# Optimization experiments

Measured on AMD Instinct MI355X. Metric: run time of the kernel, lower is better.

The kernel has to match this reference:

```python
import jax, jax.numpy as jnp
import numpy as np

N = 30000   # nodes
E = 600000  # edges (avg degree 20)
H = 128     # hidden_channels
L = 4       # num_layers
G = 64      # graphs in batch


def _init(key, shape, fan_in):
    return (jax.random.normal(key, shape, jnp.float32) / np.sqrt(fan_in)).astype(jnp.float32)


def setup_inputs() -> dict:
    key = jax.random.key(0)
    ks = jax.random.split(key, 24)
    x = jax.random.normal(ks[0], (N, 1), jnp.float32)
    pos = jax.random.normal(ks[1], (N, 3), jnp.float32)
    edge_index = jax.random.randint(ks[2], (2, E), 0, N, dtype=jnp.int32).astype(jnp.int64)
    batch = jnp.sort(jax.random.randint(ks[3], (N,), 0, G, dtype=jnp.int32)).astype(jnp.int64)

    emb_w = _init(ks[4], (1, H), 1)
    emb_b = jnp.zeros((H,), jnp.float32)

    # stacked per-layer params: msg MLP (2H+1 -> H -> H), node MLP (2H -> H -> H)
    msg_w1 = _init(ks[5], (L, 2 * H + 1, H), 2 * H + 1)
    msg_b1 = jnp.zeros((L, H), jnp.float32)
    msg_w2 = _init(ks[6], (L, H, H), H)
    msg_b2 = jnp.zeros((L, H), jnp.float32)
    node_w1 = _init(ks[7], (L, 2 * H, H), 2 * H)
    node_b1 = jnp.zeros((L, H), jnp.float32)
    node_w2 = _init(ks[8], (L, H, H), H)
    node_b2 = jnp.zeros((L, H), jnp.float32)

    out_w1 = _init(ks[9], (H, 32), H)
    out_b1 = jnp.zeros((32,), jnp.float32)
    out_w2 = _init(ks[10], (32, 1), 32)
    out_b2 = jnp.zeros((1,), jnp.float32)

    return {
        "x": x, "pos": pos, "edge_index": edge_index, "batch": batch,
        "emb_w": emb_w, "emb_b": emb_b,
        "msg_w1": msg_w1, "msg_b1": msg_b1, "msg_w2": msg_w2, "msg_b2": msg_b2,
        "node_w1": node_w1, "node_b1": node_b1, "node_w2": node_w2, "node_b2": node_b2,
        "out_w1": out_w1, "out_b1": out_b1, "out_w2": out_w2, "out_b2": out_b2,
    }


def reference(x, pos, edge_index, batch,
              emb_w, emb_b,
              msg_w1, msg_b1, msg_w2, msg_b2,
              node_w1, node_b1, node_w2, node_b2,
              out_w1, out_b1, out_w2, out_b2):
    row, col = edge_index[0], edge_index[1]  # row = source j, col = target i
    # edge scalar: squared distance (computed once, reused across layers)
    dist_sq = jnp.sum((pos[row] - pos[col]) ** 2, axis=-1, keepdims=True)  # [E,1]

    h = x @ emb_w + emb_b  # [N,H]
    for l in range(L):
        x_j = h[row]   # source features
        x_i = h[col]   # target features
        m = jnp.concatenate([x_i, x_j, dist_sq], axis=-1)           # [E, 2H+1]
        m = jax.nn.silu(m @ msg_w1[l] + msg_b1[l]) @ msg_w2[l] + msg_b2[l]  # [E,H]
        aggr = jax.ops.segment_sum(m, col, num_segments=N)          # scatter-add to targets
        nh = jnp.concatenate([h, aggr], axis=-1)                    # [N, 2H]
        h = jax.nn.silu(nh @ node_w1[l] + node_b1[l]) @ node_w2[l] + node_b2[l]
        # dropout omitted for deterministic reference (eval mode)

    g = jax.ops.segment_sum(h, batch, num_segments=G)               # global_add_pool [G,H]
    return jax.nn.silu(g @ out_w1 + out_b1) @ out_w2 + out_b2       # [G,1]
```

## Files before the change

### kernel.cpp

```cpp
#include <hip/hip_runtime.h>

typedef unsigned short u16;
typedef __bf16 bf16x8 __attribute__((ext_vector_type(8)));
typedef float f32x4 __attribute__((ext_vector_type(4)));

#define HN 128
#define TM 64
#define ASTRIDE 136
#define ECH 256

__device__ __forceinline__ u16 f2bf(float f) {
  union { float f; unsigned u; } v; v.f = f;
  unsigned r = v.u + 0x7fffu + ((v.u >> 16) & 1u);
  return (u16)(r >> 16);
}
__device__ __forceinline__ float bf2f(u16 v) {
  union { unsigned u; float f; } x; x.u = ((unsigned)v) << 16; return x.f;
}
__device__ __forceinline__ float bflo(unsigned v) {
  union { unsigned u; float f; } x; x.u = v << 16; return x.f;
}
__device__ __forceinline__ float bfhi(unsigned v) {
  union { unsigned u; float f; } x; x.u = v & 0xffff0000u; return x.f;
}
__device__ __forceinline__ float silu_f(float x) {
  float e = __builtin_amdgcn_exp2f(-1.442695041f * x);
  return x * __builtin_amdgcn_rcpf(1.f + e);
}

__global__ void pack_weights(const float* __restrict__ msg_w1, const float* __restrict__ msg_w2,
                             const float* __restrict__ node_w1, const float* __restrict__ node_w2,
                             u16* __restrict__ pw, int* __restrict__ deg,
                             float* __restrict__ g, int N_, int GH) {
  int id = blockIdx.x * 256 + threadIdx.x;
  if (id < N_) deg[id] = 0;
  if (id < GH) g[id] = 0.f;
  if (id >= 4 * 6 * 16384) return;
  int l = id / (6 * 16384);
  int rem = id % (6 * 16384);
  int m = rem / 16384;
  int e = rem % 16384;
  int kg = e >> 10;
  int n = (e >> 3) & 127;
  int j = e & 7;
  int k = kg * 8 + j;
  float v = 0.f;
  switch (m) {
    case 0: v = msg_w1[(l * 257 + k) * 128 + n]; break;
    case 1: v = msg_w1[(l * 257 + 128 + k) * 128 + n]; break;
    case 2: v = msg_w2[(l * 128 + k) * 128 + n]; break;
    case 3: v = node_w1[(l * 256 + k) * 128 + n]; break;
    case 4: v = node_w1[(l * 256 + 128 + k) * 128 + n]; break;
    case 5: v = node_w2[(l * 128 + k) * 128 + n]; break;
  }
  pw[id] = f2bf(v);
}

__device__ __forceinline__ void gemm64(const u16* s_A, const u16* s_W,
                                       int w, int quad, int m16, f32x4 acc[8]) {
#pragma unroll
  for (int ks = 0; ks < 4; ks++) {
    bf16x8 a = *(const bf16x8*)&s_A[(w * 16 + m16) * ASTRIDE + ks * 32 + quad * 8];
#pragma unroll
    for (int ct = 0; ct < 8; ct++) {
      bf16x8 b = *(const bf16x8*)&s_W[(ks * 4 + quad) * 1024 + (ct * 16 + m16) * 8];
      acc[ct] = __builtin_amdgcn_mfma_f32_16x16x32_bf16(a, b, acc[ct], 0, 0, 0);
    }
  }
}

__global__ __launch_bounds__(256) void fold_kernel(
    const float* __restrict__ msg_w2, const float* __restrict__ node_w1,
    const float* __restrict__ msg_b2, const u16* __restrict__ pw,
    u16* __restrict__ pwc, float* __restrict__ vc) {
  __shared__ __align__(16) u16 s_A[TM * ASTRIDE];
  __shared__ __align__(16) u16 s_W[16384];
  const int t = threadIdx.x;
  const int w = t >> 6, lane = t & 63, quad = lane >> 4, m16 = lane & 15;
  const int b = blockIdx.x, l = b >> 1, half = b & 1;
  const int tile0 = half * 64;

  {
    int r = t >> 2, qo = (t & 3) * 32;
    const float4* src = (const float4*)(msg_w2 + (size_t)(l * 128 + tile0 + r) * 128 + qo);
    u16* dst = s_A + r * ASTRIDE + qo;
#pragma unroll
    for (int i = 0; i < 8; i++) {
      float4 v = src[i];
      ushort4 o;
      o.x = f2bf(v.x); o.y = f2bf(v.y); o.z = f2bf(v.z); o.w = f2bf(v.w);
      *(ushort4*)(dst + i * 4) = o;
    }
  }
  {
    const int4* src = (const int4*)(pw + (size_t)(l * 6 + 4) * 16384);
    int4* dst = (int4*)s_W;
#pragma unroll
    for (int i = 0; i < 8; i++) dst[t + i * 256] = src[t + i * 256];
  }
  __syncthreads();
  f32x4 acc[8];
#pragma unroll
  for (int ct = 0; ct < 8; ct++) acc[ct] = {0.f, 0.f, 0.f, 0.f};
  gemm64(s_A, s_W, w, quad, m16, acc);
#pragma unroll
  for (int ct = 0; ct < 8; ct++)
#pragma unroll
    for (int j = 0; j < 4; j++) {
      int k = tile0 + w * 16 + quad * 4 + j;
      int n = ct * 16 + m16;
      pwc[(size_t)l * 16384 + (k >> 3) * 1024 + n * 8 + (k & 7)] = f2bf(acc[ct][j]);
    }
  if (half == 0 && t < 128) {
    float s = 0.f;
    for (int np = 0; np < 128; np++)
      s += msg_b2[l * 128 + np] * node_w1[(size_t)(l * 256 + 128 + np) * 128 + t];
    vc[l * 128 + t] = s;
  }
}

__global__ void hist_kernel(const int* __restrict__ eidx, int* __restrict__ deg,
                            int* __restrict__ rnk, int E_) {
  int e = blockIdx.x * 256 + threadIdx.x;
  if (e < E_) rnk[e] = atomicAdd(&deg[eidx[E_ + e]], 1);
}

__global__ void scan1_kernel(const int* __restrict__ deg, int* __restrict__ off,
                             int* __restrict__ bsum, int n) {
  __shared__ int s[256];
  int t = threadIdx.x;
  int i = blockIdx.x * 256 + t;
  int v = (i < n) ? deg[i] : 0;
  s[t] = v;
  for (int d = 1; d < 256; d <<= 1) {
    __syncthreads();
    int x = (t >= d) ? s[t - d] : 0;
    __syncthreads();
    s[t] += x;
  }
  __syncthreads();
  if (i < n) off[i] = s[t] - v;
  if (t == 255) bsum[blockIdx.x] = s[255];
}

__global__ void scan2_kernel(int* __restrict__ bsum, int nb) {
  __shared__ int s[256];
  int t = threadIdx.x;
  int v = (t < nb) ? bsum[t] : 0;
  s[t] = v;
  for (int d = 1; d < 256; d <<= 1) {
    __syncthreads();
    int x = (t >= d) ? s[t - d] : 0;
    __syncthreads();
    s[t] += x;
  }
  __syncthreads();
  if (t < nb) bsum[t] = s[t] - v;
}

__global__ void scan3_kernel(int* __restrict__ off, const int* __restrict__ bsum, int n) {
  int i = blockIdx.x * 256 + threadIdx.x;
  if (i < n) off[i] += bsum[blockIdx.x];
}

__global__ void scatter_kernel(const int* __restrict__ eidx, const float* __restrict__ pos,
                               const int* __restrict__ off, const int* __restrict__ rnk,
                               int2* __restrict__ es8, int E_) {
  int e = blockIdx.x * 256 + threadIdx.x;
  if (e >= E_) return;
  int sr = eidx[e], tg = eidx[E_ + e];
  float dx = pos[sr * 3 + 0] - pos[tg * 3 + 0];
  float dy = pos[sr * 3 + 1] - pos[tg * 3 + 1];
  float dz = pos[sr * 3 + 2] - pos[tg * 3 + 2];
  float d = dx * dx + dy * dy + dz * dz;
  int p = off[tg] + rnk[e];
  int2 v;
  v.x = sr | (tg << 15);
  v.y = __float_as_int(d);
  es8[p] = v;
}

__global__ __launch_bounds__(256) void proj_kernel(
    const float* __restrict__ x, const float* __restrict__ emb_w,
    const float* __restrict__ emb_b, u16* __restrict__ hbf,
    u16* __restrict__ Pout, u16* __restrict__ Qout,
    const u16* __restrict__ pw, const float* __restrict__ b1,
    float* __restrict__ S, int NH4, int nblocks, int nnodes) {
  __shared__ __align__(16) u16 s_A[TM * ASTRIDE];
  __shared__ __align__(16) u16 s_W[16384];
  const int t = threadIdx.x;
  const int w = t >> 6, lane = t & 63, quad = lane >> 4, m16 = lane & 15;
  const int tile0 = blockIdx.x * TM;

  int4 wq[8];
  {
    const int4* src = (const int4*)pw;
#pragma unroll
    for (int i = 0; i < 8; i++) wq[i] = src[t + i * 256];
  }
  __builtin_amdgcn_sched_barrier(0);
  {
    float4* S4 = (float4*)S;
    int id = blockIdx.x * 256 + t;
    int stride = nblocks * 256;
    float4 z = {0.f, 0.f, 0.f, 0.f};
    for (int i = id; i < NH4; i += stride) S4[i] = z;
  }
  {
    int r = t >> 2, qo = (t & 3) * 32;
    int node = tile0 + r;
    if (node >= nnodes) node = nnodes - 1;
    float xv = x[node];
    u16 hv[32];
#pragma unroll
    for (int i = 0; i < 32; i++) hv[i] = f2bf(xv * emb_w[qo + i] + emb_b[qo + i]);
    u16* dst = s_A + r * ASTRIDE + qo;
#pragma unroll
    for (int i = 0; i < 4; i++) *(int4*)(dst + i * 8) = *(int4*)(hv + i * 8);
    u16* gd = hbf + (size_t)node * HN + qo;
#pragma unroll
    for (int i = 0; i < 4; i++) *(int4*)(gd + i * 8) = *(int4*)(hv + i * 8);
  }
  {
    int4* dst = (int4*)s_W;
#pragma unroll
    for (int i = 0; i < 8; i++) dst[t + i * 256] = wq[i];
  }
  __syncthreads();
  {
    const int4* src = (const int4*)(pw + 16384);
#pragma unroll
    for (int i = 0; i < 8; i++) wq[i] = src[t + i * 256];
  }
  __builtin_amdgcn_sched_barrier(0);
  f32x4 acc[8];
#pragma unroll
  for (int ct = 0; ct < 8; ct++) acc[ct] = {0.f, 0.f, 0.f, 0.f};
  gemm64(s_A, s_W, w, quad, m16, acc);
  __syncthreads();
  {
    int4* dst = (int4*)s_W;
#pragma unroll
    for (int i = 0; i < 8; i++) dst[t + i * 256] = wq[i];
  }
  float bb[8];
#pragma unroll
  for (int ct = 0; ct < 8; ct++) bb[ct] = b1[ct * 16 + m16];
#pragma unroll
  for (int ct = 0; ct < 8; ct++)
#pragma unroll
    for (int j = 0; j < 4; j++) {
      int n = tile0 + w * 16 + quad * 4 + j;
      if (n < nnodes) Pout[n * HN + ct * 16 + m16] = f2bf(acc[ct][j] + bb[ct]);
    }
  __syncthreads();
#pragma unroll
  for (int ct = 0; ct < 8; ct++) acc[ct] = {0.f, 0.f, 0.f, 0.f};
  gemm64(s_A, s_W, w, quad, m16, acc);
#pragma unroll
  for (int ct = 0; ct < 8; ct++)
#pragma unroll
    for (int j = 0; j < 4; j++) {
      int n = tile0 + w * 16 + quad * 4 + j;
      if (n < nnodes) Qout[n * HN + ct * 16 + m16] = f2bf(acc[ct][j]);
    }
}

__device__ __forceinline__ void edge_step(
    int tg_s, float dd_s, unsigned qv,
    int& cur_s, float& p0, float& p1, float& s0, float& s1,
    const u16* __restrict__ P, float* __restrict__ S, int cp,
    float wd0, float wd1, int tprev_s, int tnext_s) {
  if (tg_s != cur_s) {
    if (cur_s >= 0) {
      float* dst = &S[(size_t)cur_s * HN + cp];
      if (cur_s == tprev_s || cur_s == tnext_s) {
        atomicAdd(dst, s0);
        atomicAdd(dst + 1, s1);
      } else {
        float2 v = {s0, s1};
        *(float2*)dst = v;
      }
    }
    cur_s = tg_s; s0 = 0.f; s1 = 0.f;
    int cg = tg_s < 0 ? 0 : tg_s;
    unsigned pv = *(const unsigned*)&P[(size_t)cg * HN + cp];
    p0 = bflo(pv); p1 = bfhi(pv);
  }
  float x0 = p0 + bflo(qv) + dd_s * wd0;
  float x1 = p1 + bfhi(qv) + dd_s * wd1;
  s0 += silu_f(x0);
  s1 += silu_f(x1);
}

__global__ __launch_bounds__(256) void edge_kernel(
    const u16* __restrict__ P, const u16* __restrict__ Q,
    float* __restrict__ S, const float* __restrict__ w1d,
    const int2* __restrict__ es8, int E_) {
  __shared__ int s_src[ECH + 8];
  __shared__ int s_tgt[ECH + 8];
  __shared__ float s_dist[ECH + 8];

  const int t = threadIdx.x;
  const int e0 = blockIdx.x * ECH;
  {
    int e = e0 + t;
    if (e < E_) {
      int2 v = es8[e];
      s_src[t] = v.x & 0x7fff;
      s_tgt[t] = v.x >> 15;
      s_dist[t] = __int_as_float(v.y);
    } else {
      s_src[t] = 0; s_tgt[t] = -1; s_dist[t] = 0.f;
    }
    if (t < 8) { s_src[ECH + t] = 0; s_tgt[ECH + t] = -1; s_dist[ECH + t] = 0.f; }
  }
  __syncthreads();

  const int lane = t & 63;
  const int w = t >> 6;
  const int cp = lane * 2;
  const int a = w * 64;
  const float2 wdv = *(const float2*)&w1d[cp];
  const float wd0 = wdv.x, wd1 = wdv.y;

  int tprev_s, tnext_s;
  if (w == 0) tprev_s = (e0 > 0) ? (es8[e0 - 1].x >> 15) : -2;
  else tprev_s = s_tgt[a - 1];
  if (w == 3) tnext_s = (e0 + ECH < E_) ? (es8[e0 + ECH].x >> 15) : -2;
  else tnext_s = s_tgt[a + 64];
  tprev_s = __builtin_amdgcn_readfirstlane(tprev_s);
  tnext_s = __builtin_amdgcn_readfirstlane(tnext_s);

  int tg[8];
  float dd[8];
  unsigned qv[8];
#pragma unroll
  for (int j = 0; j < 8; j++) {
    tg[j] = s_tgt[a + j];
    dd[j] = s_dist[a + j];
    qv[j] = *(const unsigned*)&Q[(size_t)s_src[a + j] * HN + cp];
  }

  int cur_s = -1;
  float s0 = 0.f, s1 = 0.f, p0 = 0.f, p1 = 0.f;

#pragma unroll
  for (int i = a; i < a + 64; i += 8) {
    int tgn[8];
    float ddn[8];
    unsigned qvn[8];
#pragma unroll
    for (int j = 0; j < 8; j++) {
      int idx = i + 8 + j;
      tgn[j] = s_tgt[idx];
      ddn[j] = s_dist[idx];
      qvn[j] = *(const unsigned*)&Q[(size_t)s_src[idx] * HN + cp];
    }
#pragma unroll
    for (int j = 0; j < 8; j++) {
      int tg_s = __builtin_amdgcn_readfirstlane(tg[j]);
      edge_step(tg_s, dd[j], qv[j], cur_s, p0, p1, s0, s1, P, S, cp, wd0, wd1, tprev_s, tnext_s);
    }
#pragma unroll
    for (int j = 0; j < 8; j++) { tg[j] = tgn[j]; dd[j] = ddn[j]; qv[j] = qvn[j]; }
  }

  if (cur_s >= 0) {
    float* dst = &S[(size_t)cur_s * HN + cp];
    if (cur_s == tprev_s || cur_s == tnext_s) {
      atomicAdd(dst, s0);
      atomicAdd(dst + 1, s1);
    } else {
      float2 v = {s0, s1};
      *(float2*)dst = v;
    }
  }
}

template <bool FUSE>
__global__ __launch_bounds__(256) void node_kernel(
    const u16* __restrict__ hbf, float* __restrict__ S, const int* __restrict__ deg,
    u16* __restrict__ hout, const u16* __restrict__ pwc, const float* __restrict__ vc,
    const u16* __restrict__ pwn, const float* __restrict__ b1, const float* __restrict__ b2,
    const u16* __restrict__ pw_next, const float* __restrict__ b1_next,
    u16* __restrict__ Pout, u16* __restrict__ Qout, int nnodes) {
  __shared__ __align__(16) u16 s_A[TM * ASTRIDE];
  __shared__ __align__(16) u16 s_W[16384];
  const int t = threadIdx.x;
  const int w = t >> 6, lane = t & 63, quad = lane >> 4, m16 = lane & 15;
  const int tile0 = blockIdx.x * TM;
  const int r_ = t >> 2, qo_ = (t & 3) * 32;
  int node_ = tile0 + r_;
  if (node_ >= nnodes) node_ = nnodes - 1;

  int4 wq[8];
  {
    const int4* src = (const int4*)pwc;
#pragma unroll
    for (int i = 0; i < 8; i++) wq[i] = src[t + i * 256];
  }
  __builtin_amdgcn_sched_barrier(0);
  {
    const float4* src = (const float4*)(S + (size_t)node_ * HN + qo_);
    u16* dst = s_A + r_ * ASTRIDE + qo_;
#pragma unroll
    for (int i = 0; i < 8; i++) {
      float4 v = src[i];
      ushort4 o;
      o.x = f2bf(v.x); o.y = f2bf(v.y); o.z = f2bf(v.z); o.w = f2bf(v.w);
      *(ushort4*)(dst + i * 4) = o;
    }
    float4 z = {0.f, 0.f, 0.f, 0.f};
    float4* zd = (float4*)(S + (size_t)node_ * HN + qo_);
#pragma unroll
    for (int i = 0; i < 8; i++) zd[i] = z;
  }
  {
    int4* dst = (int4*)s_W;
#pragma unroll
    for (int i = 0; i < 8; i++) dst[t + i * 256] = wq[i];
  }
  __syncthreads();

  int4 ha[4];
  {
    const int4* srca = (const int4*)(hbf + (size_t)node_ * HN + qo_);
#pragma unroll
    for (int i = 0; i < 4; i++) ha[i] = srca[i];
    const int4* srcw = (const int4*)pwn;
#pragma unroll
    for (int i = 0; i < 8; i++) wq[i] = srcw[t + i * 256];
  }
  __builtin_amdgcn_sched_barrier(0);
  f32x4 acc[8];
#pragma unroll
  for (int ct = 0; ct < 8; ct++) acc[ct] = {0.f, 0.f, 0.f, 0.f};
  gemm64(s_A, s_W, w, quad, m16, acc);
  __syncthreads();
  {
    int4* dsta = (int4*)(s_A + r_ * ASTRIDE + qo_);
#pragma unroll
    for (int i = 0; i < 4; i++) dsta[i] = ha[i];
    int4* dstw = (int4*)s_W;
#pragma unroll
    for (int i = 0; i < 8; i++) dstw[t + i * 256] = wq[i];
  }
  __syncthreads();

  {
    const int4* srcw = (const int4*)(pwn + 32768);
#pragma unroll
    for (int i = 0; i < 8; i++) wq[i] = srcw[t + i * 256];
  }
  __builtin_amdgcn_sched_barrier(0);
  gemm64(s_A, s_W, w, quad, m16, acc);
  __syncthreads();
  {
    int4* dstw = (int4*)s_W;
#pragma unroll
    for (int i = 0; i < 8; i++) dstw[t + i * 256] = wq[i];
  }
  if (FUSE) {
    const int4* srcw = (const int4*)pw_next;
#pragma unroll
    for (int i = 0; i < 8; i++) wq[i] = srcw[t + i * 256];
    __builtin_amdgcn_sched_barrier(0);
  }
  {
    float bb1[8], vcr[8];
#pragma unroll
    for (int ct = 0; ct < 8; ct++) {
      bb1[ct] = b1[ct * 16 + m16];
      vcr[ct] = vc[ct * 16 + m16];
    }
    float degv[4];
#pragma unroll
    for (int j = 0; j < 4; j++) {
      int n = tile0 + w * 16 + quad * 4 + j;
      if (n >= nnodes) n = nnodes - 1;
      degv[j] = (float)deg[n];
    }
#pragma unroll
    for (int ct = 0; ct < 8; ct++)
#pragma unroll
      for (int j = 0; j < 4; j++) {
        int row = w * 16 + quad * 4 + j;
        float xv = acc[ct][j] + bb1[ct] + degv[j] * vcr[ct];
        s_A[row * ASTRIDE + ct * 16 + m16] = f2bf(silu_f(xv));
      }
  }
  __syncthreads();

#pragma unroll
  for (int ct = 0; ct < 8; ct++) acc[ct] = {0.f, 0.f, 0.f, 0.f};
  gemm64(s_A, s_W, w, quad, m16, acc);

  float bb2[8];
#pragma unroll
  for (int ct = 0; ct < 8; ct++) bb2[ct] = b2[ct * 16 + m16];
#pragma unroll
  for (int ct = 0; ct < 8; ct++)
#pragma unroll
    for (int j = 0; j < 4; j++) {
      int row = w * 16 + quad * 4 + j;
      int n = tile0 + row;
      if (n < nnodes) hout[n * HN + ct * 16 + m16] = f2bf(acc[ct][j] + bb2[ct]);
    }

  if (FUSE) {
    __syncthreads();
    {
      int4* dstw = (int4*)s_W;
#pragma unroll
      for (int i = 0; i < 8; i++) dstw[t + i * 256] = wq[i];
    }
#pragma unroll
    for (int ct = 0; ct < 8; ct++)
#pragma unroll
      for (int j = 0; j < 4; j++) {
        int row = w * 16 + quad * 4 + j;
        s_A[row * ASTRIDE + ct * 16 + m16] = f2bf(acc[ct][j] + bb2[ct]);
      }
    {
      const int4* srcw = (const int4*)(pw_next + 16384);
#pragma unroll
      for (int i = 0; i < 8; i++) wq[i] = srcw[t + i * 256];
    }
    __builtin_amdgcn_sched_barrier(0);
    __syncthreads();
#pragma unroll
    for (int ct = 0; ct < 8; ct++) acc[ct] = {0.f, 0.f, 0.f, 0.f};
    gemm64(s_A, s_W, w, quad, m16, acc);
    {
      float bbn[8];
#pragma unroll
      for (int ct = 0; ct < 8; ct++) bbn[ct] = b1_next[ct * 16 + m16];
#pragma unroll
      for (int ct = 0; ct < 8; ct++)
#pragma unroll
        for (int j = 0; j < 4; j++) {
          int n = tile0 + w * 16 + quad * 4 + j;
          if (n < nnodes) Pout[n * HN + ct * 16 + m16] = f2bf(acc[ct][j] + bbn[ct]);
        }
    }
    __syncthreads();
    {
      int4* dstw = (int4*)s_W;
#pragma unroll
      for (int i = 0; i < 8; i++) dstw[t + i * 256] = wq[i];
    }
    __syncthreads();
#pragma unroll
    for (int ct = 0; ct < 8; ct++) acc[ct] = {0.f, 0.f, 0.f, 0.f};
    gemm64(s_A, s_W, w, quad, m16, acc);
#pragma unroll
    for (int ct = 0; ct < 8; ct++)
#pragma unroll
      for (int j = 0; j < 4; j++) {
        int n = tile0 + w * 16 + quad * 4 + j;
        if (n < nnodes) Qout[n * HN + ct * 16 + m16] = f2bf(acc[ct][j]);
      }
  }
}

__global__ __launch_bounds__(256) void pool_kernel(
    const u16* __restrict__ h, const int* __restrict__ batch,
    float* __restrict__ g, int N) {
  __shared__ int s_b[64];
  const int t = threadIdx.x;
  const int n0 = blockIdx.x * 64;
  if (t < 64) {
    int n = n0 + t;
    s_b[t] = (n < N) ? batch[n] : -1;
  }
  __syncthreads();
  const int cp = (t & 63) * 2;
  const int rg = t >> 6;
  int cur = -1;
  float s0 = 0.f, s1 = 0.f;
#pragma unroll 4
  for (int i = 0; i < 16; i++) {
    int r = rg * 16 + i;
    int b = s_b[r];
    if (b < 0) break;
    if (b != cur) {
      if (cur >= 0) {
        atomicAdd(&g[cur * HN + cp], s0);
        atomicAdd(&g[cur * HN + cp + 1], s1);
      }
      cur = b; s0 = 0.f; s1 = 0.f;
    }
    unsigned v = *(const unsigned*)&h[(size_t)(n0 + r) * HN + cp];
    s0 += bf2f((u16)(v & 0xffffu));
    s1 += bf2f((u16)(v >> 16));
  }
  if (cur >= 0) {
    atomicAdd(&g[cur * HN + cp], s0);
    atomicAdd(&g[cur * HN + cp + 1], s1);
  }
}

__global__ __launch_bounds__(64) void out_kernel(
    const float* __restrict__ g, const float* __restrict__ w1,
    const float* __restrict__ b1, const float* __restrict__ w2,
    const float* __restrict__ b2, float* __restrict__ out) {
  const int gi = blockIdx.x;
  const int t = threadIdx.x;
  const int c = t & 31, kh = t >> 5;
  float s = 0.f;
  for (int k = kh * 64; k < kh * 64 + 64; k++)
    s += g[gi * HN + k] * w1[k * 32 + c];
  s += __shfl_down(s, 32);
  float r = 0.f;
  if (kh == 0) r = silu_f(s + b1[c]) * w2[c];
  r += __shfl_down(r, 16);
  r += __shfl_down(r, 8);
  r += __shfl_down(r, 4);
  r += __shfl_down(r, 2);
  r += __shfl_down(r, 1);
  if (t == 0) out[gi] = r + b2[0];
}

extern "C" void kernel_launch(void* const* d_in, const int* in_sizes, int n_in,
                              void* d_out, int out_size, void* d_ws, size_t ws_size,
                              hipStream_t stream) {
  const float* x = (const float*)d_in[0];
  const float* pos = (const float*)d_in[1];
  const int* eidx = (const int*)d_in[2];
  const int* batch = (const int*)d_in[3];
  const float* emb_w = (const float*)d_in[4];
  const float* emb_b = (const float*)d_in[5];
  const float* msg_w1 = (const float*)d_in[6];
  const float* msg_b1 = (const float*)d_in[7];
  const float* msg_w2 = (const float*)d_in[8];
  const float* msg_b2 = (const float*)d_in[9];
  const float* node_w1 = (const float*)d_in[10];
  const float* node_b1 = (const float*)d_in[11];
  const float* node_w2 = (const float*)d_in[12];
  const float* node_b2 = (const float*)d_in[13];
  const float* out_w1 = (const float*)d_in[14];
  const float* out_b1 = (const float*)d_in[15];
  const float* out_w2 = (const float*)d_in[16];
  const float* out_b2 = (const float*)d_in[17];
  float* outp = (float*)d_out;

  const int N = 30000, E = 600000, G = 64;
  const size_t NH = (size_t)N * HN;

  u16* hA = (u16*)d_ws;
  u16* hB = hA + NH;
  u16* Pp = hB + NH;
  u16* Qp = Pp + NH;
  float* S = (float*)(Qp + NH);
  int2* es8 = (int2*)(S + NH);
  int* deg = (int*)(es8 + E);
  int* off = deg + N;
  int* bsum = off + N;
  float* g = (float*)(bsum + 128);
  u16* pw = (u16*)(g + G * HN);
  u16* pwc = pw + (size_t)4 * 6 * 16384;
  float* vcb = (float*)(pwc + (size_t)4 * 16384);
  int* rnk = (int*)S;

  const int NB = (N + 255) / 256;
  const int NTB = (N + TM - 1) / TM;

  pack_weights<<<(4 * 6 * 16384 + 255) / 256, 256, 0, stream>>>(
      msg_w1, msg_w2, node_w1, node_w2, pw, deg, g, N, G * HN);
  fold_kernel<<<8, 256, 0, stream>>>(msg_w2, node_w1, msg_b2, pw, pwc, vcb);

  hist_kernel<<<(E + 255) / 256, 256, 0, stream>>>(eidx, deg, rnk, E);
  scan1_kernel<<<NB, 256, 0, stream>>>(deg, off, bsum, N);
  scan2_kernel<<<1, 256, 0, stream>>>(bsum, NB);
  scan3_kernel<<<NB, 256, 0, stream>>>(off, bsum, N);
  scatter_kernel<<<(E + 255) / 256, 256, 0, stream>>>(eidx, pos, off, rnk, es8, E);

  proj_kernel<<<NTB, 256, 0, stream>>>(x, emb_w, emb_b, hA, Pp, Qp, pw, msg_b1,
                                       S, (int)(NH / 4), NTB, N);

  u16* hcur = hA;
  u16* hnext = hB;
  for (int l = 0; l < 4; l++) {
    const u16* pwl = pw + (size_t)(l * 6) * 16384;
    edge_kernel<<<(E + ECH - 1) / ECH, 256, 0, stream>>>(
        Pp, Qp, S,
        msg_w1 + (size_t)(l * 257 + 256) * 128,
        es8, E);
    if (l < 3) {
      const u16* pw_next = pw + (size_t)((l + 1) * 6) * 16384;
      node_kernel<true><<<NTB, 256, 0, stream>>>(
          hcur, S, deg, hnext, pwc + (size_t)l * 16384, vcb + l * 128,
          pwl + 3 * 16384, node_b1 + l * 128, node_b2 + l * 128,
          pw_next, msg_b1 + (l + 1) * 128, Pp, Qp, N);
    } else {
      node_kernel<false><<<NTB, 256, 0, stream>>>(
          hcur, S, deg, hnext, pwc + (size_t)l * 16384, vcb + l * 128,
          pwl + 3 * 16384, node_b1 + l * 128, node_b2 + l * 128,
          nullptr, nullptr, nullptr, nullptr, N);
    }
    u16* tmp = hcur; hcur = hnext; hnext = tmp;
  }

  pool_kernel<<<(N + 63) / 64, 256, 0, stream>>>(hcur, batch, g, N);
  out_kernel<<<G, 64, 0, stream>>>(g, out_w1, out_b1, out_w2, out_b2, outp);
}
```

Measured before the change: 468.7 us.

## Make proj and node kernels persistent with all layer weights resident in LDS

The proj and node kernels become persistent grids of 256 blocks that loop over 64-node tiles. Each block loads all its weight matrices into shared memory once, up to four 32 KB matrices, instead of reloading and swapping a single weight buffer per tile. A and H operands are fed from registers or straight from global memory where possible. Block-wide barriers are replaced by per-wave lgkmcnt waits, since each wave works only on its own rows. In exchange, the large LDS footprint limits occupancy to one block per CU, and the last GEMM reads its weights directly from global memory.

```diff
diff --git a/kernel.cpp b/kernel.cpp
--- a/kernel.cpp
+++ b/kernel.cpp
@@ -8,6 +8,7 @@
 #define TM 64
 #define ASTRIDE 136
 #define ECH 256
+#define PGRID 256
 
 __device__ __forceinline__ u16 f2bf(float f) {
   union { float f; unsigned u; } v; v.f = f;
@@ -69,6 +70,31 @@
   }
 }
 
+__device__ __forceinline__ void gemm64_ra(const bf16x8 aH[4], const u16* s_W,
+                                          int quad, int m16, f32x4 acc[8]) {
+#pragma unroll
+  for (int ks = 0; ks < 4; ks++) {
+#pragma unroll
+    for (int ct = 0; ct < 8; ct++) {
+      bf16x8 b = *(const bf16x8*)&s_W[(ks * 4 + quad) * 1024 + (ct * 16 + m16) * 8];
+      acc[ct] = __builtin_amdgcn_mfma_f32_16x16x32_bf16(aH[ks], b, acc[ct], 0, 0, 0);
+    }
+  }
+}
+
+__device__ __forceinline__ void gemm64_gb(const u16* s_A, const u16* __restrict__ gW,
+                                          int w, int quad, int m16, f32x4 acc[8]) {
+#pragma unroll
+  for (int ks = 0; ks < 4; ks++) {
+    bf16x8 a = *(const bf16x8*)&s_A[(w * 16 + m16) * ASTRIDE + ks * 32 + quad * 8];
+#pragma unroll
+    for (int ct = 0; ct < 8; ct++) {
+      bf16x8 b = *(const bf16x8*)&gW[(ks * 4 + quad) * 1024 + (ct * 16 + m16) * 8];
+      acc[ct] = __builtin_amdgcn_mfma_f32_16x16x32_bf16(a, b, acc[ct], 0, 0, 0);
+    }
+  }
+}
+
 __global__ __launch_bounds__(256) void fold_kernel(
     const float* __restrict__ msg_w2, const float* __restrict__ node_w1,
     const float* __restrict__ msg_b2, const u16* __restrict__ pw,
@@ -180,90 +206,82 @@
   es8[p] = v;
 }
 
-__global__ __launch_bounds__(256) void proj_kernel(
+__global__ __launch_bounds__(256, 1) void proj_kernel(
     const float* __restrict__ x, const float* __restrict__ emb_w,
     const float* __restrict__ emb_b, u16* __restrict__ hbf,
     u16* __restrict__ Pout, u16* __restrict__ Qout,
     const u16* __restrict__ pw, const float* __restrict__ b1,
-    float* __restrict__ S, int NH4, int nblocks, int nnodes) {
-  __shared__ __align__(16) u16 s_A[TM * ASTRIDE];
-  __shared__ __align__(16) u16 s_W[16384];
+    float* __restrict__ S, int NH4, int nnodes, int ntiles) {
+  __shared__ __align__(16) u16 s_W[2 * 16384];
   const int t = threadIdx.x;
   const int w = t >> 6, lane = t & 63, quad = lane >> 4, m16 = lane & 15;
-  const int tile0 = blockIdx.x * TM;
-
-  int4 wq[8];
-  {
-    const int4* src = (const int4*)pw;
-#pragma unroll
-    for (int i = 0; i < 8; i++) wq[i] = src[t + i * 256];
-  }
-  __builtin_amdgcn_sched_barrier(0);
+
   {
     float4* S4 = (float4*)S;
     int id = blockIdx.x * 256 + t;
-    int stride = nblocks * 256;
+    int stride = PGRID * 256;
     float4 z = {0.f, 0.f, 0.f, 0.f};
     for (int i = id; i < NH4; i += stride) S4[i] = z;
   }
   {
-    int r = t >> 2, qo = (t & 3) * 32;
-    int node = tile0 + r;
-    if (node >= nnodes) node = nnodes - 1;
-    float xv = x[node];
-    u16 hv[32];
-#pragma unroll
-    for (int i = 0; i < 32; i++) hv[i] = f2bf(xv * emb_w[qo + i] + emb_b[qo + i]);
-    u16* dst = s_A + r * ASTRIDE + qo;
-#pragma unroll
-    for (int i = 0; i < 4; i++) *(int4*)(dst + i * 8) = *(int4*)(hv + i * 8);
-    u16* gd = hbf + (size_t)node * HN + qo;
-#pragma unroll
-    for (int i = 0; i < 4; i++) *(int4*)(gd + i * 8) = *(int4*)(hv + i * 8);
-  }
-  {
+    const int4* src0 = (const int4*)pw;
+    const int4* src1 = (const int4*)(pw + 16384);
     int4* dst = (int4*)s_W;
 #pragma unroll
-    for (int i = 0; i < 8; i++) dst[t + i * 256] = wq[i];
-  }
+    for (int i = 0; i < 8; i++) dst[t + i * 256] = src0[t + i * 256];
+#pragma unroll
+    for (int i = 0; i < 8; i++) dst[2048 + t + i * 256] = src1[t + i * 256];
+  }
+  float ew[4][8], eb[4][8], bb[8];
+#pragma unroll
+  for (int ks = 0; ks < 4; ks++)
+#pragma unroll
+    for (int i = 0; i < 8; i++) {
+      int c = ks * 32 + quad * 8 + i;
+      ew[ks][i] = emb_w[c];
+      eb[ks][i] = emb_b[c];
+    }
+#pragma unroll
+  for (int ct = 0; ct < 8; ct++) bb[ct] = b1[ct * 16 + m16];
   __syncthreads();
-  {
-    const int4* src = (const int4*)(pw + 16384);
-#pragma unroll
-    for (int i = 0; i < 8; i++) wq[i] = src[t + i * 256];
-  }
-  __builtin_amdgcn_sched_barrier(0);
-  f32x4 acc[8];
-#pragma unroll
-  for (int ct = 0; ct < 8; ct++) acc[ct] = {0.f, 0.f, 0.f, 0.f};
-  gemm64(s_A, s_W, w, quad, m16, acc);
-  __syncthreads();
-  {
-    int4* dst = (int4*)s_W;
-#pragma unroll
-    for (int i = 0; i < 8; i++) dst[t + i * 256] = wq[i];
-  }
-  float bb[8];
-#pragma unroll
-  for (int ct = 0; ct < 8; ct++) bb[ct] = b1[ct * 16 + m16];
-#pragma unroll
-  for (int ct = 0; ct < 8; ct++)
-#pragma unroll
-    for (int j = 0; j < 4; j++) {
-      int n = tile0 + w * 16 + quad * 4 + j;
-      if (n < nnodes) Pout[n * HN + ct * 16 + m16] = f2bf(acc[ct][j] + bb[ct]);
-    }
-  __syncthreads();
-#pragma unroll
-  for (int ct = 0; ct < 8; ct++) acc[ct] = {0.f, 0.f, 0.f, 0.f};
-  gemm64(s_A, s_W, w, quad, m16, acc);
-#pragma unroll
-  for (int ct = 0; ct < 8; ct++)
-#pragma unroll
-    for (int j = 0; j < 4; j++) {
-      int n = tile0 + w * 16 + quad * 4 + j;
-      if (n < nnodes) Qout[n * HN + ct * 16 + m16] = f2bf(acc[ct][j]);
-    }
+
+  for (int tile = blockIdx.x; tile < ntiles; tile += PGRID) {
+    const int tile0 = tile * TM;
+    int nodem = tile0 + w * 16 + m16;
+    bool live = nodem < nnodes;
+    if (!live) nodem = nnodes - 1;
+    float xv = x[nodem];
+    bf16x8 aH[4];
+#pragma unroll
+    for (int ks = 0; ks < 4; ks++) {
+      u16 hv[8];
+#pragma unroll
+      for (int i = 0; i < 8; i++) hv[i] = f2bf(xv * ew[ks][i] + eb[ks][i]);
+      aH[ks] = *(bf16x8*)hv;
+      if (live) *(int4*)&hbf[(size_t)nodem * HN + ks * 32 + quad * 8] = *(int4*)hv;
+    }
+    f32x4 acc[8];
+#pragma unroll
+    for (int ct = 0; ct < 8; ct++) acc[ct] = {0.f, 0.f, 0.f, 0.f};
+    gemm64_ra(aH, s_W, quad, m16, acc);
+#pragma unroll
+    for (int ct = 0; ct < 8; ct++)
+#pragma unroll
+      for (int j = 0; j < 4; j++) {
+        int n = tile0 + w * 16 + quad * 4 + j;
+        if (n < nnodes) Pout[(size_t)n * HN + ct * 16 + m16] = f2bf(acc[ct][j] + bb[ct]);
+      }
+#pragma unroll
+    for (int ct = 0; ct < 8; ct++) acc[ct] = {0.f, 0.f, 0.f, 0.f};
+    gemm64_ra(aH, s_W + 16384, quad, m16, acc);
+#pragma unroll
+    for (int ct = 0; ct < 8; ct++)
+#pragma unroll
+      for (int j = 0; j < 4; j++) {
+        int n = tile0 + w * 16 + quad * 4 + j;
+        if (n < nnodes) Qout[(size_t)n * HN + ct * 16 + m16] = f2bf(acc[ct][j]);
+      }
+  }
 }
 
 __device__ __forceinline__ void edge_step(
@@ -379,188 +397,137 @@
 }
 
 template <bool FUSE>
-__global__ __launch_bounds__(256) void node_kernel(
+__global__ __launch_bounds__(256, 1) void node_kernel(
     const u16* __restrict__ hbf, float* __restrict__ S, const int* __restrict__ deg,
     u16* __restrict__ hout, const u16* __restrict__ pwc, const float* __restrict__ vc,
     const u16* __restrict__ pwn, const float* __restrict__ b1, const float* __restrict__ b2,
     const u16* __restrict__ pw_next, const float* __restrict__ b1_next,
-    u16* __restrict__ Pout, u16* __restrict__ Qout, int nnodes) {
+    u16* __restrict__ Pout, u16* __restrict__ Qout, int nnodes, int ntiles) {
   __shared__ __align__(16) u16 s_A[TM * ASTRIDE];
-  __shared__ __align__(16) u16 s_W[16384];
+  __shared__ __align__(16) u16 s_W[(FUSE ? 4 : 3) * 16384];
   const int t = threadIdx.x;
   const int w = t >> 6, lane = t & 63, quad = lane >> 4, m16 = lane & 15;
-  const int tile0 = blockIdx.x * TM;
   const int r_ = t >> 2, qo_ = (t & 3) * 32;
-  int node_ = tile0 + r_;
-  if (node_ >= nnodes) node_ = nnodes - 1;
-
-  int4 wq[8];
+
   {
-    const int4* src = (const int4*)pwc;
-#pragma unroll
-    for (int i = 0; i < 8; i++) wq[i] = src[t + i * 256];
-  }
-  __builtin_amdgcn_sched_barrier(0);
-  {
-    const float4* src = (const float4*)(S + (size_t)node_ * HN + qo_);
-    u16* dst = s_A + r_ * ASTRIDE + qo_;
-#pragma unroll
-    for (int i = 0; i < 8; i++) {
-      float4 v = src[i];
-      ushort4 o;
-      o.x = f2bf(v.x); o.y = f2bf(v.y); o.z = f2bf(v.z); o.w = f2bf(v.w);
-      *(ushort4*)(dst + i * 4) = o;
-    }
-    float4 z = {0.f, 0.f, 0.f, 0.f};
-    float4* zd = (float4*)(S + (size_t)node_ * HN + qo_);
-#pragma unroll
-    for (int i = 0; i < 8; i++) zd[i] = z;
-  }
-  {
+    const int4* src0 = (const int4*)pwc;
+    const int4* src1 = (const int4*)pwn;
+    const int4* src2 = (const int4*)(pwn + 32768);
     int4* dst = (int4*)s_W;
 #pragma unroll
-    for (int i = 0; i < 8; i++) dst[t + i * 256] = wq[i];
+    for (int i = 0; i < 8; i++) dst[t + i * 256] = src0[t + i * 256];
+#pragma unroll
+    for (int i = 0; i < 8; i++) dst[2048 + t + i * 256] = src1[t + i * 256];
+#pragma unroll
+    for (int i = 0; i < 8; i++) dst[4096 + t + i * 256] = src2[t + i * 256];
+    if (FUSE) {
+      const int4* src3 = (const int4*)pw_next;
+#pragma unroll
+      for (int i = 0; i < 8; i++) dst[6144 + t + i * 256] = src3[t + i * 256];
+    }
+  }
+  float bb1[8], vcr[8], bb2[8], bbn[8];
+#pragma unroll
+  for (int ct = 0; ct < 8; ct++) {
+    bb1[ct] = b1[ct * 16 + m16];
+    vcr[ct] = vc[ct * 16 + m16];
+    bb2[ct] = b2[ct * 16 + m16];
+    bbn[ct] = FUSE ? b1_next[ct * 16 + m16] : 0.f;
   }
   __syncthreads();
 
-  int4 ha[4];
-  {
-    const int4* srca = (const int4*)(hbf + (size_t)node_ * HN + qo_);
-#pragma unroll
-    for (int i = 0; i < 4; i++) ha[i] = srca[i];
-    const int4* srcw = (const int4*)pwn;
-#pragma unroll
-    for (int i = 0; i < 8; i++) wq[i] = srcw[t + i * 256];
-  }
-  __builtin_amdgcn_sched_barrier(0);
-  f32x4 acc[8];
-#pragma unroll
-  for (int ct = 0; ct < 8; ct++) acc[ct] = {0.f, 0.f, 0.f, 0.f};
-  gemm64(s_A, s_W, w, quad, m16, acc);
-  __syncthreads();
-  {
-    int4* dsta = (int4*)(s_A + r_ * ASTRIDE + qo_);
-#pragma unroll
-    for (int i = 0; i < 4; i++) dsta[i] = ha[i];
-    int4* dstw = (int4*)s_W;
-#pragma unroll
-    for (int i = 0; i < 8; i++) dstw[t + i * 256] = wq[i];
-  }
-  __syncthreads();
-
-  {
-    const int4* srcw = (const int4*)(pwn + 32768);
-#pragma unroll
-    for (int i = 0; i < 8; i++) wq[i] = srcw[t + i * 256];
-  }
-  __builtin_amdgcn_sched_barrier(0);
-  gemm64(s_A, s_W, w, quad, m16, acc);
-  __syncthreads();
-  {
-    int4* dstw = (int4*)s_W;
-#pragma unroll
-    for (int i = 0; i < 8; i++) dstw[t + i * 256] = wq[i];
-  }
-  if (FUSE) {
-    const int4* srcw = (const int4*)pw_next;
-#pragma unroll
-    for (int i = 0; i < 8; i++) wq[i] = srcw[t + i * 256];
-    __builtin_amdgcn_sched_barrier(0);
-  }
-  {
-    float bb1[8], vcr[8];
-#pragma unroll
-    for (int ct = 0; ct < 8; ct++) {
-      bb1[ct] = b1[ct * 16 + m16];
-      vcr[ct] = vc[ct * 16 + m16];
-    }
-    float degv[4];
-#pragma unroll
-    for (int j = 0; j < 4; j++) {
-      int n = tile0 + w * 16 + quad * 4 + j;
-      if (n >= nnodes) n = nnodes - 1;
-      degv[j] = (float)deg[n];
-    }
+  for (int tile = blockIdx.x; tile < ntiles; tile += PGRID) {
+    const int tile0 = tile * TM;
+    int node_ = tile0 + r_;
+    if (node_ >= nnodes) node_ = nnodes - 1;
+    int nodem = tile0 + w * 16 + m16;
+    if (nodem >= nnodes) nodem = nnodes - 1;
+
+    {
+      const float4* src = (const float4*)(S + (size_t)node_ * HN + qo_);
+      u16* dst = s_A + r_ * ASTRIDE + qo_;
+#pragma unroll
+      for (int i = 0; i < 8; i++) {
+        float4 v = src[i];
+        ushort4 o;
+        o.x = f2bf(v.x); o.y = f2bf(v.y); o.z = f2bf(v.z); o.w = f2bf(v.w);
+        *(ushort4*)(dst + i * 4) = o;
+      }
+      float4 z = {0.f, 0.f, 0.f, 0.f};
+      float4* zd = (float4*)(S + (size_t)node_ * HN + qo_);
+#pragma unroll
+      for (int i = 0; i < 8; i++) zd[i] = z;
+    }
+    asm volatile("s_waitcnt lgkmcnt(0)" ::: "memory");
+
+    f32x4 acc[8];
+#pragma unroll
+    for (int ct = 0; ct < 8; ct++) acc[ct] = {0.f, 0.f, 0.f, 0.f};
+    gemm64(s_A, s_W, w, quad, m16, acc);
+
+    bf16x8 aH[4];
+#pragma unroll
+    for (int ks = 0; ks < 4; ks++)
+      aH[ks] = *(const bf16x8*)&hbf[(size_t)nodem * HN + ks * 32 + quad * 8];
+    gemm64_ra(aH, s_W + 16384, quad, m16, acc);
+
+    {
+      float degv[4];
+#pragma unroll
+      for (int j = 0; j < 4; j++) {
+        int n = tile0 + w * 16 + quad * 4 + j;
+        if (n >= nnodes) n = nnodes - 1;
+        degv[j] = (float)deg[n];
+      }
+#pragma unroll
+      for (int ct = 0; ct < 8; ct++)
+#pragma unroll
+        for (int j = 0; j < 4; j++) {
+          int row = w * 16 + quad * 4 + j;
+          float xv = acc[ct][j] + bb1[ct] + degv[j] * vcr[ct];
+          s_A[row * ASTRIDE + ct * 16 + m16] = f2bf(silu_f(xv));
+        }
+    }
+    asm volatile("s_waitcnt lgkmcnt(0)" ::: "memory");
+
+#pragma unroll
+    for (int ct = 0; ct < 8; ct++) acc[ct] = {0.f, 0.f, 0.f, 0.f};
+    gemm64(s_A, s_W + 32768, w, quad, m16, acc);
+
 #pragma unroll
     for (int ct = 0; ct < 8; ct++)
 #pragma unroll
       for (int j = 0; j < 4; j++) {
         int row = w * 16 + quad * 4 + j;
-        float xv = acc[ct][j] + bb1[ct] + degv[j] * vcr[ct];
-        s_A[row * ASTRIDE + ct * 16 + m16] = f2bf(silu_f(xv));
+        int n = tile0 + row;
+        u16 hv = f2bf(acc[ct][j] + bb2[ct]);
+        if (n < nnodes) hout[(size_t)n * HN + ct * 16 + m16] = hv;
+        if (FUSE) s_A[row * ASTRIDE + ct * 16 + m16] = hv;
       }
-  }
-  __syncthreads();
-
-#pragma unroll
-  for (int ct = 0; ct < 8; ct++) acc[ct] = {0.f, 0.f, 0.f, 0.f};
-  gemm64(s_A, s_W, w, quad, m16, acc);
-
-  float bb2[8];
-#pragma unroll
-  for (int ct = 0; ct < 8; ct++) bb2[ct] = b2[ct * 16 + m16];
-#pragma unroll
-  for (int ct = 0; ct < 8; ct++)
-#pragma unroll
-    for (int j = 0; j < 4; j++) {
-      int row = w * 16 + quad * 4 + j;
-      int n = tile0 + row;
-      if (n < nnodes) hout[n * HN + ct * 16 + m16] = f2bf(acc[ct][j] + bb2[ct]);
-    }
-
-  if (FUSE) {
-    __syncthreads();
-    {
-      int4* dstw = (int4*)s_W;
-#pragma unroll
-      for (int i = 0; i < 8; i++) dstw[t + i * 256] = wq[i];
-    }
-#pragma unroll
-    for (int ct = 0; ct < 8; ct++)
-#pragma unroll
-      for (int j = 0; j < 4; j++) {
-        int row = w * 16 + quad * 4 + j;
-        s_A[row * ASTRIDE + ct * 16 + m16] = f2bf(acc[ct][j] + bb2[ct]);
-      }
-    {
-      const int4* srcw = (const int4*)(pw_next + 16384);
-#pragma unroll
-      for (int i = 0; i < 8; i++) wq[i] = srcw[t + i * 256];
-    }
-    __builtin_amdgcn_sched_barrier(0);
-    __syncthreads();
-#pragma unroll
-    for (int ct = 0; ct < 8; ct++) acc[ct] = {0.f, 0.f, 0.f, 0.f};
-    gemm64(s_A, s_W, w, quad, m16, acc);
-    {
-      float bbn[8];
-#pragma unroll
-      for (int ct = 0; ct < 8; ct++) bbn[ct] = b1_next[ct * 16 + m16];
+
+    if (FUSE) {
+      asm volatile("s_waitcnt lgkmcnt(0)" ::: "memory");
+#pragma unroll
+      for (int ct = 0; ct < 8; ct++) acc[ct] = {0.f, 0.f, 0.f, 0.f};
+      gemm64(s_A, s_W + 49152, w, quad, m16, acc);
 #pragma unroll
       for (int ct = 0; ct < 8; ct++)
 #pragma unroll
         for (int j = 0; j < 4; j++) {
           int n = tile0 + w * 16 + quad * 4 + j;
-          if (n < nnodes) Pout[n * HN + ct * 16 + m16] = f2bf(acc[ct][j] + bbn[ct]);
+          if (n < nnodes) Pout[(size_t)n * HN + ct * 16 + m16] = f2bf(acc[ct][j] + bbn[ct]);
         }
-    }
-    __syncthreads();
-    {
-      int4* dstw = (int4*)s_W;
-#pragma unroll
-      for (int i = 0; i < 8; i++) dstw[t + i * 256] = wq[i];
-    }
-    __syncthreads();
-#pragma unroll
-    for (int ct = 0; ct < 8; ct++) acc[ct] = {0.f, 0.f, 0.f, 0.f};
-    gemm64(s_A, s_W, w, quad, m16, acc);
-#pragma unroll
-    for (int ct = 0; ct < 8; ct++)
-#pragma unroll
-      for (int j = 0; j < 4; j++) {
-        int n = tile0 + w * 16 + quad * 4 + j;
-        if (n < nnodes) Qout[n * HN + ct * 16 + m16] = f2bf(acc[ct][j]);
-      }
+#pragma unroll
+      for (int ct = 0; ct < 8; ct++) acc[ct] = {0.f, 0.f, 0.f, 0.f};
+      gemm64_gb(s_A, pw_next + 16384, w, quad, m16, acc);
+#pragma unroll
+      for (int ct = 0; ct < 8; ct++)
+#pragma unroll
+        for (int j = 0; j < 4; j++) {
+          int n = tile0 + w * 16 + quad * 4 + j;
+          if (n < nnodes) Qout[(size_t)n * HN + ct * 16 + m16] = f2bf(acc[ct][j]);
+        }
+    }
   }
 }
 
@@ -676,8 +643,8 @@
   scan3_kernel<<<NB, 256, 0, stream>>>(off, bsum, N);
   scatter_kernel<<<(E + 255) / 256, 256, 0, stream>>>(eidx, pos, off, rnk, es8, E);
 
-  proj_kernel<<<NTB, 256, 0, stream>>>(x, emb_w, emb_b, hA, Pp, Qp, pw, msg_b1,
-                                       S, (int)(NH / 4), NTB, N);
+  proj_kernel<<<PGRID, 256, 0, stream>>>(x, emb_w, emb_b, hA, Pp, Qp, pw, msg_b1,
+                                         S, (int)(NH / 4), N, NTB);
 
   u16* hcur = hA;
   u16* hnext = hB;
@@ -689,15 +656,15 @@
         es8, E);
     if (l < 3) {
       const u16* pw_next = pw + (size_t)((l + 1) * 6) * 16384;
-      node_kernel<true><<<NTB, 256, 0, stream>>>(
+      node_kernel<true><<<PGRID, 256, 0, stream>>>(
           hcur, S, deg, hnext, pwc + (size_t)l * 16384, vcb + l * 128,
           pwl + 3 * 16384, node_b1 + l * 128, node_b2 + l * 128,
-          pw_next, msg_b1 + (l + 1) * 128, Pp, Qp, N);
+          pw_next, msg_b1 + (l + 1) * 128, Pp, Qp, N, NTB);
     } else {
-      node_kernel<false><<<NTB, 256, 0, stream>>>(
+      node_kernel<false><<<PGRID, 256, 0, stream>>>(
           hcur, S, deg, hnext, pwc + (size_t)l * 16384, vcb + l * 128,
           pwl + 3 * 16384, node_b1 + l * 128, node_b2 + l * 128,
-          nullptr, nullptr, nullptr, nullptr, N);
+          nullptr, nullptr, nullptr, nullptr, N, NTB);
     }
     u16* tmp = hcur; hcur = hnext; hnext = tmp;
   }
```

Result: faster. 420.2 us (-10.4%).
